# Performance work log

Measured on AMD Instinct MI355X. Metric: run time of the kernel, lower is better.

Reference implementation:

```python
import jax, jax.numpy as jnp
import numpy as np

# Mamba3TextEncoder config (class .small() defaults)
B_SZ, SEQ = 4, 512
VOCAB, D_MODEL, N_LAYERS = 32000, 768, 12
N_STATE, EXPAND, HEADDIM, NGROUPS, EMBED = 64, 2, 32, 1, 1536
D_INNER = EXPAND * D_MODEL            # 1536
NHEADS = D_INNER // HEADDIM           # 48
CONV_DIM = D_INNER + 2 * NGROUPS * N_STATE  # 1664 (x, B, C go through depthwise conv)
K_CONV = 4
PROJ_IN = 2 * D_INNER + 2 * NGROUPS * N_STATE + NHEADS  # z, xBC, dt


def setup_inputs() -> dict:
    key = jax.random.key(0)
    ks = jax.random.split(key, 16)
    s = 0.02
    return {
        "token_ids": jax.random.randint(ks[0], (B_SZ, SEQ), 0, VOCAB),
        "embed_W": jax.random.normal(ks[1], (VOCAB, D_MODEL), jnp.float32) * s,
        "ln_W": jnp.ones((N_LAYERS, D_MODEL), jnp.float32),
        "in_proj_W": jax.random.normal(ks[2], (N_LAYERS, D_MODEL, PROJ_IN), jnp.float32) * s,
        "conv_W": jax.random.normal(ks[3], (N_LAYERS, CONV_DIM, 1, K_CONV), jnp.float32) * 0.1,
        "conv_b": jnp.zeros((N_LAYERS, CONV_DIM), jnp.float32),
        "dt_bias": jax.random.uniform(ks[4], (N_LAYERS, NHEADS), jnp.float32, -4.6, -2.0),
        "A_log": jnp.tile(jnp.log(jnp.arange(1, NHEADS + 1, dtype=jnp.float32))[None], (N_LAYERS, 1)),
        "D": jnp.ones((N_LAYERS, NHEADS), jnp.float32),
        "norm_W": jnp.ones((N_LAYERS, D_INNER), jnp.float32),
        "out_proj_W": jax.random.normal(ks[5], (N_LAYERS, D_INNER, D_MODEL), jnp.float32) * s,
        "final_norm_W": jnp.ones((D_MODEL,), jnp.float32),
        "proj_W": jax.random.normal(ks[6], (D_MODEL, EMBED), jnp.float32) * s,
        "proj_b": jnp.zeros((EMBED,), jnp.float32),
    }


def _rmsnorm(x, w, eps=1e-5):
    return x * jax.lax.rsqrt(jnp.mean(x * x, axis=-1, keepdims=True) + eps) * w


def _causal_conv(x, w, b):
    # x: [B,S,C] depthwise causal conv, kernel K_CONV
    y = jax.lax.conv_general_dilated(
        x.transpose(0, 2, 1), w, (1,), [(K_CONV - 1, 0)],
        dimension_numbers=("NCH", "OIH", "NCH"), feature_group_count=CONV_DIM)
    return y.transpose(0, 2, 1) + b


def _ssm(xs, dt, A, Bm, Cm):
    # selective scan. xs:[B,S,H,P] dt:[B,S,H] A:[H] Bm,Cm:[B,S,N] (ngroups=1)
    decay = jnp.exp(dt * A)              # [B,S,H]
    dtx = dt[..., None] * xs             # [B,S,H,P]
    h0 = jnp.zeros((xs.shape[0], NHEADS, HEADDIM, N_STATE), xs.dtype)

    def step(h, inp):
        dec, dx, b, c = inp              # [B,H],[B,H,P],[B,N],[B,N]
        h = dec[..., None, None] * h + dx[..., None] * b[:, None, None, :]
        y = jnp.einsum("bhpn,bn->bhp", h, c)
        return h, y

    inputs = (decay.transpose(1, 0, 2), dtx.transpose(1, 0, 2, 3),
              Bm.transpose(1, 0, 2), Cm.transpose(1, 0, 2))
    _, ys = jax.lax.scan(step, h0, inputs)
    return ys.transpose(1, 0, 2, 3)      # [B,S,H,P]


def reference(token_ids, embed_W, ln_W, in_proj_W, conv_W, conv_b, dt_bias,
              A_log, D, norm_W, out_proj_W, final_norm_W, proj_W, proj_b):
    x = embed_W[token_ids]                               # [B,S,D]
    for l in range(N_LAYERS):
        h = _rmsnorm(x, ln_W[l])
        zxbcdt = h @ in_proj_W[l]                        # [B,S,PROJ_IN]
        z = zxbcdt[..., :D_INNER]
        xBC = zxbcdt[..., D_INNER:D_INNER + CONV_DIM]
        dt_raw = zxbcdt[..., D_INNER + CONV_DIM:]        # [B,S,H]
        xBC = jax.nn.silu(_causal_conv(xBC, conv_W[l], conv_b[l]))
        xs = xBC[..., :D_INNER].reshape(*xBC.shape[:2], NHEADS, HEADDIM)
        Bm = xBC[..., D_INNER:D_INNER + N_STATE]
        Cm = xBC[..., D_INNER + N_STATE:]
        dt = jax.nn.softplus(dt_raw + dt_bias[l])
        A = -jnp.exp(A_log[l])
        y = _ssm(xs, dt, A, Bm, Cm) + D[l][None, None, :, None] * xs
        y = y.reshape(*y.shape[:2], D_INNER)
        y = _rmsnorm(y * jax.nn.silu(z), norm_W[l])      # gated RMSNorm
        x = x + y @ out_proj_W[l]
    x = _rmsnorm(x, final_norm_W)
    pooled = x.mean(axis=1)                              # [B,D]
    proj = pooled @ proj_W + proj_b                      # [B,EMBED]
    n = jnp.sqrt(jnp.sum(proj * proj, axis=-1, keepdims=True))
    return proj / jnp.maximum(n, 1e-12)
```

## Files before the change

### kernel.cpp

```cpp
#include <hip/hip_runtime.h>
#include <math.h>

typedef __bf16 bf16x8 __attribute__((ext_vector_type(8)));
typedef short  s16x8  __attribute__((ext_vector_type(8)));
typedef float  f32x4  __attribute__((ext_vector_type(4)));

static constexpr int BSZ = 4, SEQ = 512, DM = 768;
static constexpr int DIN = 1536, NH = 48, HP = 32, NS = 64;
static constexpr int CDIM = 1664;
static constexpr int PROJ_IN = 3248;
static constexpr int LDZX = 3328;
static constexpr int ROWS = BSZ * SEQ;
static constexpr int EMBED = 1536;
static constexpr int NLAYERS = 12;

using gptr_t = const __attribute__((address_space(1))) void*;
using lptr_t = __attribute__((address_space(3))) void*;

__device__ __forceinline__ unsigned short f2bf(float f) {
  unsigned u = __builtin_bit_cast(unsigned, f);
  u += 0x7FFF + ((u >> 16) & 1);
  return (unsigned short)(u >> 16);
}
__device__ __forceinline__ float bf2f(unsigned short u) {
  unsigned v = (unsigned)u << 16;
  return __builtin_bit_cast(float, v);
}
__device__ __forceinline__ float sigm(float x) { return 1.f / (1.f + __expf(-x)); }
__device__ __forceinline__ float sp(float x) { return (x > 15.f) ? x : log1pf(__expf(x)); }

__device__ __forceinline__ void gll16(const void* g, void* l) {
  __builtin_amdgcn_global_load_lds((gptr_t)g, (lptr_t)l, 16, 0, 0);
}
__device__ __forceinline__ f32x4 mfma16(s16x8 a, s16x8 b, f32x4 c) {
  return __builtin_amdgcn_mfma_f32_16x16x32_bf16(
      __builtin_bit_cast(bf16x8, a), __builtin_bit_cast(bf16x8, b), c, 0, 0, 0);
}

template <int NW>
__device__ __forceinline__ float block_sum(float v) {
#pragma unroll
  for (int o = 32; o; o >>= 1) v += __shfl_xor(v, o);
  __shared__ float red[NW];
  if ((threadIdx.x & 63) == 0) red[threadIdx.x >> 6] = v;
  __syncthreads();
  float s = red[0];
#pragma unroll
  for (int i = 1; i < NW; ++i) s += red[i];
  return s;
}

__global__ void embed_k(const int* __restrict__ tok, const float* __restrict__ eW,
                        float* __restrict__ x) {
  int bt = blockIdx.x;
  const float4* src = (const float4*)(eW + (size_t)tok[bt] * DM);
  float4* dst = (float4*)(x + (size_t)bt * DM);
  dst[threadIdx.x] = src[threadIdx.x];
}

__global__ void transpose_cvt(const float* __restrict__ W, unsigned short* __restrict__ Wt,
                              int K, int N, int Npad) {
  __shared__ float tile[32][33];
  int l = blockIdx.z;
  const float* Wl = W + (size_t)l * K * N;
  unsigned short* Wtl = Wt + (size_t)l * Npad * K;
  int nb = blockIdx.x * 32, kb = blockIdx.y * 32;
  int tx = threadIdx.x, ty = threadIdx.y;
#pragma unroll
  for (int r = 0; r < 4; ++r) {
    int k = kb + ty + r * 8, n = nb + tx;
    tile[ty + r * 8][tx] = (n < N) ? Wl[(size_t)k * N + n] : 0.f;
  }
  __syncthreads();
#pragma unroll
  for (int r = 0; r < 4; ++r) {
    int n = nb + ty + r * 8, k = kb + tx;
    Wtl[(size_t)n * K + k] = f2bf(tile[tx][ty + r * 8]);
  }
}

template <typename OUT>
__global__ void rmsnorm_k(const float* __restrict__ x, const float* __restrict__ w,
                          OUT* __restrict__ out) {
  int bt = blockIdx.x, tid = threadIdx.x;
  float4 v = ((const float4*)(x + (size_t)bt * DM))[tid];
  float4 wv = ((const float4*)w)[tid];
  float ss = v.x * v.x + v.y * v.y + v.z * v.z + v.w * v.w;
  float tot = block_sum<3>(ss);
  float rs = rsqrtf(tot * (1.f / DM) + 1e-5f);
  float o0 = v.x * rs * wv.x, o1 = v.y * rs * wv.y, o2 = v.z * rs * wv.z, o3 = v.w * rs * wv.w;
  if constexpr (sizeof(OUT) == 4) {
    float4 o = {o0, o1, o2, o3};
    ((float4*)(out + (size_t)bt * DM))[tid] = o;
  } else {
    unsigned long long pk =
        (unsigned long long)f2bf(o0) | ((unsigned long long)f2bf(o1) << 16) |
        ((unsigned long long)f2bf(o2) << 32) | ((unsigned long long)f2bf(o3) << 48);
    *(unsigned long long*)((unsigned short*)out + (size_t)bt * DM + tid * 4) = pk;
  }
}

template <int BM, int BN, int MODE>
__global__ __launch_bounds__(256) void gemm_k(
    const unsigned short* __restrict__ A, const unsigned short* __restrict__ Bt,
    int K, void* __restrict__ O0, void* __restrict__ O1, void* __restrict__ O2) {
  constexpr int AIT = BM / 32, BIT = BN / 32, NST = AIT + BIT;
  constexpr int FM = BM / 32, FN = BN / 32;
  __shared__ unsigned short lA[2][BM * 64], lB[2][BN * 64];
  int tid = threadIdx.x, lane = tid & 63, wv = tid >> 6;
  int flat = blockIdx.y * gridDim.x + blockIdx.x;
  int q8 = (gridDim.x * gridDim.y) >> 3;
  int nf = (flat & 7) * q8 + (flat >> 3);
  int bx = nf % gridDim.x, by = nf / gridDim.x;
  int m0 = by * BM, n0 = bx * BN;
  int wm = (wv >> 1) * (BM / 2), wn = (wv & 1) * (BN / 2);
  int NK = K >> 6;
  auto stage = [&](int kt, int buf) {
#pragma unroll
    for (int i = 0; i < AIT; ++i) {
      int flt = i * 256 + tid, rr = flt >> 3, cc = flt & 7;
      gll16(A + (size_t)(m0 + rr) * K + kt + (cc ^ (rr & 7)) * 8, (char*)lA[buf] + flt * 16);
    }
#pragma unroll
    for (int i = 0; i < BIT; ++i) {
      int flt = i * 256 + tid, rr = flt >> 3, cc = flt & 7;
      gll16(Bt + (size_t)(n0 + rr) * K + kt + (cc ^ (rr & 7)) * 8, (char*)lB[buf] + flt * 16);
    }
  };
  f32x4 acc[FM][FN] = {};
  stage(0, 0);
  for (int i = 0; i < NK; ++i) {
    if (i + 1 < NK) {
      stage((i + 1) << 6, (i + 1) & 1);
      asm volatile("s_waitcnt vmcnt(%0)" :: "i"(NST) : "memory");
    } else {
      asm volatile("s_waitcnt vmcnt(0)" ::: "memory");
    }
    __builtin_amdgcn_s_barrier();
    __builtin_amdgcn_sched_barrier(0);
    const unsigned short* cA = lA[i & 1];
    const unsigned short* cB = lB[i & 1];
#pragma unroll
    for (int ks = 0; ks < 2; ++ks) {
      s16x8 a[FM], b[FN];
#pragma unroll
      for (int mi = 0; mi < FM; ++mi) {
        int row = wm + mi * 16 + (lane & 15);
        int ch = (ks * 4 + (lane >> 4)) ^ (row & 7);
        a[mi] = *(const s16x8*)((const char*)cA + row * 128 + ch * 16);
      }
#pragma unroll
      for (int nj = 0; nj < FN; ++nj) {
        int row = wn + nj * 16 + (lane & 15);
        int ch = (ks * 4 + (lane >> 4)) ^ (row & 7);
        b[nj] = *(const s16x8*)((const char*)cB + row * 128 + ch * 16);
      }
#pragma unroll
      for (int mi = 0; mi < FM; ++mi)
#pragma unroll
        for (int nj = 0; nj < FN; ++nj)
          acc[mi][nj] = mfma16(a[mi], b[nj], acc[mi][nj]);
    }
    __builtin_amdgcn_s_barrier();
  }
#pragma unroll
  for (int mi = 0; mi < FM; ++mi) {
    int rbase = m0 + wm + mi * 16 + ((lane >> 4) << 2);
#pragma unroll
    for (int nj = 0; nj < FN; ++nj) {
      int col = n0 + wn + nj * 16 + (lane & 15);
#pragma unroll
      for (int rg = 0; rg < 4; ++rg) {
        int row = rbase + rg;
        float vv = acc[mi][nj][rg];
        if constexpr (MODE == 0) {
          if (n0 < DIN) {
            ((unsigned short*)O0)[(size_t)row * DIN + col] = f2bf(vv);
          } else if (n0 < DIN + CDIM) {
            ((float*)O1)[(size_t)row * CDIM + (col - DIN)] = vv;
          } else {
            int c2 = col - (DIN + CDIM);
            if (c2 < NH) ((float*)O2)[(size_t)row * NH + c2] = vv;
          }
        } else {
          size_t idx = (size_t)row * DM + col;
          ((float*)O0)[idx] = vv + ((const float*)O1)[idx];
        }
      }
    }
  }
}

__global__ __launch_bounds__(256) void conv_dt_k(
    const float* __restrict__ xbc, const float* __restrict__ cw, const float* __restrict__ cb,
    const float* __restrict__ dtraw, const float* __restrict__ dbias,
    unsigned short* __restrict__ xs16, unsigned short* __restrict__ dtxT,
    unsigned short* __restrict__ Bbf, unsigned short* __restrict__ Cbf) {
  __shared__ float stg[11][256];
  __shared__ float dtl[8][48];
  int tid = threadIdx.x;
  int chunk = blockIdx.x;
  int bt0 = blockIdx.y * 8;
  int t0 = bt0 & (SEQ - 1);
  int cbase = chunk * 256;
#pragma unroll
  for (int i = 0; i < 11; ++i) {
    int s = t0 - 3 + i, col = cbase + tid;
    stg[i][tid] = (s >= 0 && col < CDIM) ? xbc[(size_t)(bt0 - 3 + i) * CDIM + col] : 0.f;
  }
  if (chunk < 6) {
    for (int idx = tid; idx < 384; idx += 256) {
      int r = idx / 48, hh = idx - r * 48;
      dtl[r][hh] = sp(dtraw[(size_t)(bt0 + r) * NH + hh] + dbias[hh]);
    }
  }
  __syncthreads();
  int c = cbase + tid;
  if (chunk < 6) {
    float w0 = cw[c * 4], w1 = cw[c * 4 + 1], w2 = cw[c * 4 + 2], w3 = cw[c * 4 + 3];
    float bias = cb[c];
    int hh = c >> 5, p = c & 31, b = bt0 >> 9;
    s16x8 pk;
#pragma unroll
    for (int r = 0; r < 8; ++r) {
      float a = bias + stg[r][tid] * w0 + stg[r + 1][tid] * w1 + stg[r + 2][tid] * w2 +
                stg[r + 3][tid] * w3;
      float sv = a * sigm(a);
      xs16[(size_t)(bt0 + r) * DIN + c] = f2bf(sv);
      pk[r] = (short)f2bf(sv * dtl[r][hh]);
    }
    *reinterpret_cast<s16x8*>(dtxT + ((((size_t)b * NH + hh) * HP + p) * SEQ + t0)) = pk;
  } else if (tid < 128) {
    int cc = DIN + tid;
    float w0 = cw[cc * 4], w1 = cw[cc * 4 + 1], w2 = cw[cc * 4 + 2], w3 = cw[cc * 4 + 3];
    float bias = cb[cc];
#pragma unroll
    for (int r = 0; r < 8; ++r) {
      float a = bias + stg[r][tid] * w0 + stg[r + 1][tid] * w1 + stg[r + 2][tid] * w2 +
                stg[r + 3][tid] * w3;
      float sv = a * sigm(a);
      if (tid < 64) Bbf[(size_t)(bt0 + r) * NS + tid] = f2bf(sv);
      else          Cbf[(size_t)(bt0 + r) * NS + (tid - 64)] = f2bf(sv);
    }
  }
}

__global__ __launch_bounds__(256) void scan_k(
    const unsigned short* __restrict__ Bbf, const unsigned short* __restrict__ Cbf,
    const unsigned short* __restrict__ dtxT, const unsigned short* __restrict__ xs16,
    const float* __restrict__ dtraw, const float* __restrict__ dbias,
    const float* __restrict__ alog, const float* __restrict__ Dvec,
    unsigned short* __restrict__ y16) {
  __shared__ unsigned short CbPt[64 * 64];
  __shared__ unsigned short Bb[2][64 * 64], Dx[2][32 * 64];
  __shared__ float lsb[SEQ];
  __shared__ float pair[256];
  __shared__ int sfirst;
  int tid = threadIdx.x, lane = tid & 63, wv = tid >> 6;
  int tb = blockIdx.x, h = blockIdx.y, b = blockIdx.z;
  int t0 = tb * 64;
  const unsigned short* dxrow = dtxT + ((size_t)b * NH + h) * HP * SEQ;

#pragma unroll
  for (int i = 0; i < 2; ++i) {
    int flt = i * 256 + tid, rr = flt >> 3, cc = flt & 7;
    gll16(Cbf + (size_t)(b * SEQ + t0 + rr) * NS + (cc ^ (rr & 7)) * 8, (char*)CbPt + flt * 16);
  }
  float bias = dbias[h];
  float Ah = -__expf(alog[h]);
  int t2 = tid * 2;
  float d0 = sp(dtraw[(size_t)(b * SEQ + t2) * NH + h] + bias) * Ah;
  float d1 = sp(dtraw[(size_t)(b * SEQ + t2 + 1) * NH + h] + bias) * Ah;
  pair[tid] = d0 + d1;
  __syncthreads();
  for (int off = 1; off < 256; off <<= 1) {
    float add = (tid >= off) ? pair[tid - off] : 0.f;
    float cur = pair[tid];
    __syncthreads();
    pair[tid] = cur + add;
    __syncthreads();
  }
  float excl = tid ? pair[tid - 1] : 0.f;
  lsb[t2] = excl + d0;
  lsb[t2 + 1] = excl + d0 + d1;
  if (tid == 0) sfirst = tb;
  __syncthreads();
  float REF = lsb[t0];
  if (tid < tb && (REF - lsb[tid * 64 + 63] >= -18.f)) atomicMin(&sfirst, tid);
  __syncthreads();
  int st0 = sfirst;

#pragma unroll
  for (int i = 0; i < 2; ++i) {
    int flt = i * 256 + tid, rr = flt >> 3, cc = flt & 7;
    gll16(Bbf + (size_t)(b * SEQ + st0 * 64 + rr) * NS + (cc ^ (rr & 7)) * 8,
          (char*)Bb[st0 & 1] + flt * 16);
  }
  { int rr = tid >> 3, cc = tid & 7;
    gll16(dxrow + (size_t)rr * SEQ + st0 * 64 + (cc ^ (rr & 7)) * 8,
          (char*)Dx[st0 & 1] + tid * 16); }

  float lt[4], elt[4];
  int trb = wv * 16 + ((lane >> 4) << 2);
#pragma unroll
  for (int rg = 0; rg < 4; ++rg) {
    lt[rg] = lsb[t0 + trb + rg];
    elt[rg] = __expf(lt[rg] - REF);
  }
  s16x8 aC[2];
  f32x4 yacc[2] = {};

  for (int st = st0; st <= tb; ++st) {
    int s0 = st * 64;
    if (st < tb) {
      int s1 = s0 + 64;
#pragma unroll
      for (int i = 0; i < 2; ++i) {
        int flt = i * 256 + tid, rr = flt >> 3, cc = flt & 7;
        gll16(Bbf + (size_t)(b * SEQ + s1 + rr) * NS + (cc ^ (rr & 7)) * 8,
              (char*)Bb[(st + 1) & 1] + flt * 16);
      }
      { int rr = tid >> 3, cc = tid & 7;
        gll16(dxrow + (size_t)rr * SEQ + s1 + (cc ^ (rr & 7)) * 8,
              (char*)Dx[(st + 1) & 1] + tid * 16); }
      asm volatile("s_waitcnt vmcnt(3)" ::: "memory");
    } else {
      asm volatile("s_waitcnt vmcnt(0)" ::: "memory");
    }
    __builtin_amdgcn_s_barrier();
    __builtin_amdgcn_sched_barrier(0);
    const unsigned short* Bcur = Bb[st & 1];
    const unsigned short* Dcur = Dx[st & 1];
    if (st == st0) {
#pragma unroll
      for (int ks = 0; ks < 2; ++ks) {
        int row = wv * 16 + (lane & 15);
        int ch = (ks * 4 + (lane >> 4)) ^ (row & 7);
        aC[ks] = *(const s16x8*)((const char*)CbPt + row * 128 + ch * 16);
      }
    }
    float lsv[4];
#pragma unroll
    for (int sq = 0; sq < 4; ++sq) lsv[sq] = lsb[s0 + sq * 16 + (lane & 15)];
    f32x4 gf[4] = {};
#pragma unroll
    for (int sq = 0; sq < 4; ++sq)
#pragma unroll
      for (int ks = 0; ks < 2; ++ks) {
        int row = sq * 16 + (lane & 15);
        int ch = (ks * 4 + (lane >> 4)) ^ (row & 7);
        s16x8 bB = *(const s16x8*)((const char*)Bcur + row * 128 + ch * 16);
        gf[sq] = mfma16(aC[ks], bB, gf[sq]);
      }
    if (st < tb) {
      float es[4];
#pragma unroll
      for (int sq = 0; sq < 4; ++sq) es[sq] = __expf(REF - lsv[sq]);
#pragma unroll
      for (int sq = 0; sq < 4; ++sq) {
        int scol = sq * 16 + (lane & 15);
#pragma unroll
        for (int rg = 0; rg < 4; ++rg) {
          int trow = trb + rg;
          int off = (trow * 128 + scol * 2) ^ ((trow & 7) << 4);
          *(unsigned short*)((char*)CbPt + off) = f2bf(gf[sq][rg] * (elt[rg] * es[sq]));
        }
      }
    } else {
#pragma unroll
      for (int sq = 0; sq < 4; ++sq) {
        int scol = sq * 16 + (lane & 15);
        int sg = s0 + scol;
#pragma unroll
        for (int rg = 0; rg < 4; ++rg) {
          int trow = trb + rg, tg = t0 + trow;
          float wgt = (sg <= tg) ? __expf(lt[rg] - lsv[sq]) : 0.f;
          int off = (trow * 128 + scol * 2) ^ ((trow & 7) << 4);
          *(unsigned short*)((char*)CbPt + off) = f2bf(gf[sq][rg] * wgt);
        }
      }
    }
#pragma unroll
    for (int ks = 0; ks < 2; ++ks) {
      int row = wv * 16 + (lane & 15);
      int ch = (ks * 4 + (lane >> 4)) ^ (row & 7);
      s16x8 aP = *(const s16x8*)((const char*)CbPt + row * 128 + ch * 16);
#pragma unroll
      for (int pq = 0; pq < 2; ++pq) {
        int prow = pq * 16 + (lane & 15);
        int pch = (ks * 4 + (lane >> 4)) ^ (prow & 7);
        s16x8 bD = *(const s16x8*)((const char*)Dcur + prow * 128 + pch * 16);
        yacc[pq] = mfma16(aP, bD, yacc[pq]);
      }
    }
    __builtin_amdgcn_s_barrier();
  }
  float Dh = Dvec[h];
#pragma unroll
  for (int pq = 0; pq < 2; ++pq) {
#pragma unroll
    for (int rg = 0; rg < 4; ++rg) {
      int trow = trb + rg;
      int tg = t0 + trow;
      int p = pq * 16 + (lane & 15);
      float xv = bf2f(xs16[(size_t)(b * SEQ + tg) * DIN + h * HP + p]);
      y16[(size_t)(b * SEQ + tg) * DIN + h * HP + p] = f2bf(yacc[pq][rg] + Dh * xv);
    }
  }
}

__global__ void gated_rms_k(const unsigned short* __restrict__ y16,
                            const unsigned short* __restrict__ zb,
                            const float* __restrict__ w, unsigned short* __restrict__ out) {
  int bt = blockIdx.x, tid = threadIdx.x;
  size_t base = (size_t)bt * DIN + tid * 8;
  s16x8 yv = *(const s16x8*)(y16 + base);
  s16x8 zv = *(const s16x8*)(zb + base);
  float g[8], ss = 0.f;
#pragma unroll
  for (int j = 0; j < 8; ++j) {
    float yf = bf2f((unsigned short)yv[j]), zf = bf2f((unsigned short)zv[j]);
    float gg = yf * zf * sigm(zf);
    g[j] = gg; ss += gg * gg;
  }
  float tot = block_sum<3>(ss);
  float rs = rsqrtf(tot * (1.f / DIN) + 1e-5f);
  s16x8 ov;
#pragma unroll
  for (int j = 0; j < 8; ++j) ov[j] = (short)f2bf(g[j] * rs * w[tid * 8 + j]);
  *(s16x8*)(out + base) = ov;
}

__global__ void pool_k(const float* __restrict__ fn, float* __restrict__ pooled) {
  int d = blockIdx.x * 256 + threadIdx.x, b = blockIdx.y;
  float s = 0.f;
  for (int t = 0; t < SEQ; ++t) s += fn[(size_t)(b * SEQ + t) * DM + d];
  pooled[b * DM + d] = s * (1.f / SEQ);
}
__global__ void proj_k(const float* __restrict__ pooled, const float* __restrict__ pW,
                       const float* __restrict__ pb, float* __restrict__ ptmp) {
  int e0 = blockIdx.x * 64, b = blockIdx.y;
  int el = threadIdx.x & 63, g = threadIdx.x >> 6;
  int e = e0 + el;
  float s = 0.f;
  for (int d = g * 192; d < (g + 1) * 192; ++d)
    s += pooled[b * DM + d] * pW[(size_t)d * EMBED + e];
  __shared__ float red[4][64];
  red[g][el] = s;
  __syncthreads();
  if (g == 0) ptmp[b * EMBED + e] = red[0][el] + red[1][el] + red[2][el] + red[3][el] + pb[e];
}
__global__ void l2_k(const float* __restrict__ ptmp, float* __restrict__ out) {
  int b = blockIdx.x;
  float v[6], ss = 0.f;
#pragma unroll
  for (int i = 0; i < 6; ++i) {
    v[i] = ptmp[(size_t)b * EMBED + threadIdx.x + i * 256];
    ss += v[i] * v[i];
  }
  float tot = block_sum<4>(ss);
  float inv = 1.f / fmaxf(sqrtf(tot), 1e-12f);
#pragma unroll
  for (int i = 0; i < 6; ++i)
    out[(size_t)b * EMBED + threadIdx.x + i * 256] = v[i] * inv;
}

extern "C" void kernel_launch(void* const* d_in, const int* in_sizes, int n_in,
                              void* d_out, int out_size, void* d_ws, size_t ws_size,
                              hipStream_t stream) {
  const int*   tok  = (const int*)d_in[0];
  const float* embW = (const float*)d_in[1];
  const float* lnW  = (const float*)d_in[2];
  const float* ipW  = (const float*)d_in[3];
  const float* cW   = (const float*)d_in[4];
  const float* cB   = (const float*)d_in[5];
  const float* dtB  = (const float*)d_in[6];
  const float* Alog = (const float*)d_in[7];
  const float* Dv   = (const float*)d_in[8];
  const float* nW   = (const float*)d_in[9];
  const float* opW  = (const float*)d_in[10];
  const float* fnW  = (const float*)d_in[11];
  const float* pW   = (const float*)d_in[12];
  const float* pb   = (const float*)d_in[13];
  float* out = (float*)d_out;

  char* wsp = (char*)d_ws;
  auto alloc = [&](size_t bytes) {
    char* p = wsp;
    wsp += (bytes + 255) & ~(size_t)255;
    return p;
  };
  float* x      = (float*)alloc((size_t)ROWS * DM * 4);
  float* xbc    = (float*)alloc((size_t)ROWS * CDIM * 4);
  float* dtraw  = (float*)alloc((size_t)ROWS * NH * 4);
  float* pooled = (float*)alloc((size_t)BSZ * DM * 4);
  float* ptmp   = (float*)alloc((size_t)BSZ * EMBED * 4);
  float* fn     = (float*)alloc((size_t)ROWS * DM * 4);
  unsigned short* zb    = (unsigned short*)alloc((size_t)ROWS * DIN * 2);
  unsigned short* xs16  = (unsigned short*)alloc((size_t)ROWS * DIN * 2);
  unsigned short* y16   = (unsigned short*)alloc((size_t)ROWS * DIN * 2);
  unsigned short* h16   = (unsigned short*)alloc((size_t)ROWS * DM * 2);
  unsigned short* yg16  = (unsigned short*)alloc((size_t)ROWS * DIN * 2);
  unsigned short* dtxT  = (unsigned short*)alloc((size_t)BSZ * NH * HP * SEQ * 2);
  unsigned short* Bbf   = (unsigned short*)alloc((size_t)ROWS * NS * 2);
  unsigned short* Cbf   = (unsigned short*)alloc((size_t)ROWS * NS * 2);
  unsigned short* wptA  = (unsigned short*)alloc((size_t)NLAYERS * LDZX * DM * 2);
  unsigned short* wotA  = (unsigned short*)alloc((size_t)NLAYERS * DM * DIN * 2);

  embed_k<<<ROWS, 192, 0, stream>>>(tok, embW, x);
  transpose_cvt<<<dim3(LDZX / 32, DM / 32, NLAYERS), dim3(32, 8), 0, stream>>>(
      ipW, wptA, DM, PROJ_IN, LDZX);
  transpose_cvt<<<dim3(DM / 32, DIN / 32, NLAYERS), dim3(32, 8), 0, stream>>>(
      opW, wotA, DIN, DM, DM);

  for (int l = 0; l < NLAYERS; ++l) {
    rmsnorm_k<unsigned short><<<ROWS, 192, 0, stream>>>(x, lnW + l * DM, h16);
    gemm_k<128, 128, 0><<<dim3(LDZX / 128, ROWS / 128), 256, 0, stream>>>(
        h16, wptA + (size_t)l * LDZX * DM, DM, zb, xbc, dtraw);
    conv_dt_k<<<dim3(7, ROWS / 8), 256, 0, stream>>>(
        xbc, cW + (size_t)l * CDIM * 4, cB + (size_t)l * CDIM, dtraw, dtB + l * NH,
        xs16, dtxT, Bbf, Cbf);
    scan_k<<<dim3(SEQ / 64, NH, BSZ), 256, 0, stream>>>(
        Bbf, Cbf, dtxT, xs16, dtraw, dtB + l * NH, Alog + l * NH, Dv + l * NH, y16);
    gated_rms_k<<<ROWS, 192, 0, stream>>>(y16, zb, nW + (size_t)l * DIN, yg16);
    gemm_k<64, 64, 1><<<dim3(DM / 64, ROWS / 64), 256, 0, stream>>>(
        yg16, wotA + (size_t)l * DM * DIN, DIN, x, x, nullptr);
  }

  rmsnorm_k<float><<<ROWS, 192, 0, stream>>>(x, fnW, fn);
  pool_k<<<dim3(DM / 256, BSZ), 256, 0, stream>>>(fn, pooled);
  proj_k<<<dim3(EMBED / 64, BSZ), 256, 0, stream>>>(pooled, pW, pb, ptmp);
  l2_k<<<BSZ, 256, 0, stream>>>(ptmp, out);
}
```

Before: 1.065 ms.

## Pre-pack GEMM operands into MFMA fragment layout and load directly to registers

Weights and activations are now written in a packed 16-row by 32-k fragment order, so each lane of the new GEMM can load its MFMA operands with a single contiguous 16-byte global load. This removes the LDS staging, swizzling and barriers of the old GEMM and replaces them with register double-buffering, at the cost of relying on L1/L2 for cross-wave reuse. The embedding lookup is fused with the first layer's RMSNorm. The scan's chunk-skip threshold is also tightened from -18 to -12, which skips more decayed history at a small accuracy cost.

```diff
diff --git a/kernel.cpp b/kernel.cpp
--- a/kernel.cpp
+++ b/kernel.cpp
@@ -50,38 +50,57 @@
   return s;
 }
 
-__global__ void embed_k(const int* __restrict__ tok, const float* __restrict__ eW,
-                        float* __restrict__ x) {
-  int bt = blockIdx.x;
-  const float4* src = (const float4*)(eW + (size_t)tok[bt] * DM);
-  float4* dst = (float4*)(x + (size_t)bt * DM);
-  dst[threadIdx.x] = src[threadIdx.x];
-}
-
-__global__ void transpose_cvt(const float* __restrict__ W, unsigned short* __restrict__ Wt,
-                              int K, int N, int Npad) {
+
+__global__ void embed_rms_k(const int* __restrict__ tok, const float* __restrict__ eW,
+                            const float* __restrict__ w, float* __restrict__ x,
+                            unsigned short* __restrict__ hpk) {
+  int bt = blockIdx.x, tid = threadIdx.x;
+  float4 v = ((const float4*)(eW + (size_t)tok[bt] * DM))[tid];
+  ((float4*)(x + (size_t)bt * DM))[tid] = v;
+  float4 wv = ((const float4*)w)[tid];
+  float ss = v.x * v.x + v.y * v.y + v.z * v.z + v.w * v.w;
+  float tot = block_sum<3>(ss);
+  float rs = rsqrtf(tot * (1.f / DM) + 1e-5f);
+  int k0 = tid * 4;
+  unsigned long long pk =
+      (unsigned long long)f2bf(v.x * rs * wv.x) |
+      ((unsigned long long)f2bf(v.y * rs * wv.y) << 16) |
+      ((unsigned long long)f2bf(v.z * rs * wv.z) << 32) |
+      ((unsigned long long)f2bf(v.w * rs * wv.w) << 48);
+  size_t idx = (((size_t)(bt >> 4) * 24 + (k0 >> 5)) * 64 +
+                ((bt & 15) | (((k0 >> 3) & 3) << 4))) * 8 + (k0 & 7);
+  *(unsigned long long*)(hpk + idx) = pk;
+}
+
+__global__ void transpose_pk(const float* __restrict__ W, unsigned short* __restrict__ Wpk,
+                             int K, int N, int Npad) {
   __shared__ float tile[32][33];
-  int l = blockIdx.z;
+  int l = blockIdx.z, KC = K >> 5;
   const float* Wl = W + (size_t)l * K * N;
-  unsigned short* Wtl = Wt + (size_t)l * Npad * K;
+  unsigned short* Wp = Wpk + (size_t)l * Npad * K;
   int nb = blockIdx.x * 32, kb = blockIdx.y * 32;
-  int tx = threadIdx.x, ty = threadIdx.y;
+  int tx = threadIdx.x & 31, ty = threadIdx.x >> 5;
 #pragma unroll
   for (int r = 0; r < 4; ++r) {
     int k = kb + ty + r * 8, n = nb + tx;
     tile[ty + r * 8][tx] = (n < N) ? Wl[(size_t)k * N + n] : 0.f;
   }
   __syncthreads();
-#pragma unroll
-  for (int r = 0; r < 4; ++r) {
-    int n = nb + ty + r * 8, k = kb + tx;
-    Wtl[(size_t)n * K + k] = f2bf(tile[tx][ty + r * 8]);
-  }
-}
-
-template <typename OUT>
+  int n_local = threadIdx.x >> 3, kg = threadIdx.x & 7;
+  int n = nb + n_local, k0 = kb + kg * 4;
+  unsigned long long pk =
+      (unsigned long long)f2bf(tile[kg * 4 + 0][n_local]) |
+      ((unsigned long long)f2bf(tile[kg * 4 + 1][n_local]) << 16) |
+      ((unsigned long long)f2bf(tile[kg * 4 + 2][n_local]) << 32) |
+      ((unsigned long long)f2bf(tile[kg * 4 + 3][n_local]) << 48);
+  size_t idx = (((size_t)(n >> 4) * KC + (k0 >> 5)) * 64 +
+                ((n & 15) | (((k0 >> 3) & 3) << 4))) * 8 + (k0 & 7);
+  *(unsigned long long*)(Wp + idx) = pk;
+}
+
+template <bool PACK>
 __global__ void rmsnorm_k(const float* __restrict__ x, const float* __restrict__ w,
-                          OUT* __restrict__ out) {
+                          void* __restrict__ out) {
   int bt = blockIdx.x, tid = threadIdx.x;
   float4 v = ((const float4*)(x + (size_t)bt * DM))[tid];
   float4 wv = ((const float4*)w)[tid];
@@ -89,82 +108,65 @@
   float tot = block_sum<3>(ss);
   float rs = rsqrtf(tot * (1.f / DM) + 1e-5f);
   float o0 = v.x * rs * wv.x, o1 = v.y * rs * wv.y, o2 = v.z * rs * wv.z, o3 = v.w * rs * wv.w;
-  if constexpr (sizeof(OUT) == 4) {
+  if constexpr (!PACK) {
     float4 o = {o0, o1, o2, o3};
-    ((float4*)(out + (size_t)bt * DM))[tid] = o;
+    ((float4*)((float*)out + (size_t)bt * DM))[tid] = o;
   } else {
+    int k0 = tid * 4;
     unsigned long long pk =
         (unsigned long long)f2bf(o0) | ((unsigned long long)f2bf(o1) << 16) |
         ((unsigned long long)f2bf(o2) << 32) | ((unsigned long long)f2bf(o3) << 48);
-    *(unsigned long long*)((unsigned short*)out + (size_t)bt * DM + tid * 4) = pk;
-  }
-}
-
-template <int BM, int BN, int MODE>
-__global__ __launch_bounds__(256) void gemm_k(
-    const unsigned short* __restrict__ A, const unsigned short* __restrict__ Bt,
-    int K, void* __restrict__ O0, void* __restrict__ O1, void* __restrict__ O2) {
-  constexpr int AIT = BM / 32, BIT = BN / 32, NST = AIT + BIT;
-  constexpr int FM = BM / 32, FN = BN / 32;
-  __shared__ unsigned short lA[2][BM * 64], lB[2][BN * 64];
+    size_t idx = (((size_t)(bt >> 4) * 24 + (k0 >> 5)) * 64 +
+                  ((bt & 15) | (((k0 >> 3) & 3) << 4))) * 8 + (k0 & 7);
+    *(unsigned long long*)((unsigned short*)out + idx) = pk;
+  }
+}
+
+template <int FN, int MODE>
+__global__ __launch_bounds__(256) void gemm_pk(
+    const unsigned short* __restrict__ Apk, const unsigned short* __restrict__ Bpk,
+    int K, void* __restrict__ O0, void* __restrict__ O1) {
+  constexpr int BN = FN * 32;
+  int KC = K >> 5;
   int tid = threadIdx.x, lane = tid & 63, wv = tid >> 6;
   int flat = blockIdx.y * gridDim.x + blockIdx.x;
   int q8 = (gridDim.x * gridDim.y) >> 3;
   int nf = (flat & 7) * q8 + (flat >> 3);
   int bx = nf % gridDim.x, by = nf / gridDim.x;
-  int m0 = by * BM, n0 = bx * BN;
-  int wm = (wv >> 1) * (BM / 2), wn = (wv & 1) * (BN / 2);
-  int NK = K >> 6;
-  auto stage = [&](int kt, int buf) {
-#pragma unroll
-    for (int i = 0; i < AIT; ++i) {
-      int flt = i * 256 + tid, rr = flt >> 3, cc = flt & 7;
-      gll16(A + (size_t)(m0 + rr) * K + kt + (cc ^ (rr & 7)) * 8, (char*)lA[buf] + flt * 16);
-    }
-#pragma unroll
-    for (int i = 0; i < BIT; ++i) {
-      int flt = i * 256 + tid, rr = flt >> 3, cc = flt & 7;
-      gll16(Bt + (size_t)(n0 + rr) * K + kt + (cc ^ (rr & 7)) * 8, (char*)lB[buf] + flt * 16);
-    }
+  int m0 = by * 128, n0 = bx * BN;
+  int wm = (wv >> 1) * 64, wn = (wv & 1) * (FN * 16);
+  int arb = (m0 + wm) >> 4, brb = (n0 + wn) >> 4;
+  const unsigned short* abase = Apk + ((size_t)arb * KC) * 512 + lane * 8;
+  const unsigned short* bbase = Bpk + ((size_t)brb * KC) * 512 + lane * 8;
+  auto lda = [&](s16x8* A, int cb) {
+#pragma unroll
+    for (int mi = 0; mi < 4; ++mi)
+      A[mi] = *(const s16x8*)(abase + ((size_t)mi * KC + cb) * 512);
   };
-  f32x4 acc[FM][FN] = {};
-  stage(0, 0);
-  for (int i = 0; i < NK; ++i) {
-    if (i + 1 < NK) {
-      stage((i + 1) << 6, (i + 1) & 1);
-      asm volatile("s_waitcnt vmcnt(%0)" :: "i"(NST) : "memory");
-    } else {
-      asm volatile("s_waitcnt vmcnt(0)" ::: "memory");
-    }
-    __builtin_amdgcn_s_barrier();
-    __builtin_amdgcn_sched_barrier(0);
-    const unsigned short* cA = lA[i & 1];
-    const unsigned short* cB = lB[i & 1];
-#pragma unroll
-    for (int ks = 0; ks < 2; ++ks) {
-      s16x8 a[FM], b[FN];
-#pragma unroll
-      for (int mi = 0; mi < FM; ++mi) {
-        int row = wm + mi * 16 + (lane & 15);
-        int ch = (ks * 4 + (lane >> 4)) ^ (row & 7);
-        a[mi] = *(const s16x8*)((const char*)cA + row * 128 + ch * 16);
-      }
-#pragma unroll
-      for (int nj = 0; nj < FN; ++nj) {
-        int row = wn + nj * 16 + (lane & 15);
-        int ch = (ks * 4 + (lane >> 4)) ^ (row & 7);
-        b[nj] = *(const s16x8*)((const char*)cB + row * 128 + ch * 16);
-      }
-#pragma unroll
-      for (int mi = 0; mi < FM; ++mi)
-#pragma unroll
-        for (int nj = 0; nj < FN; ++nj)
-          acc[mi][nj] = mfma16(a[mi], b[nj], acc[mi][nj]);
-    }
-    __builtin_amdgcn_s_barrier();
-  }
-#pragma unroll
-  for (int mi = 0; mi < FM; ++mi) {
+  auto ldb = [&](s16x8* B, int cb) {
+#pragma unroll
+    for (int nj = 0; nj < FN; ++nj)
+      B[nj] = *(const s16x8*)(bbase + ((size_t)nj * KC + cb) * 512);
+  };
+  f32x4 acc[4][FN] = {};
+  s16x8 A0[4], B0[FN], A1[4], B1[FN];
+  lda(A0, 0); ldb(B0, 0);
+  for (int cb = 0; cb < KC; cb += 2) {
+    lda(A1, cb + 1); ldb(B1, cb + 1);
+#pragma unroll
+    for (int mi = 0; mi < 4; ++mi)
+#pragma unroll
+      for (int nj = 0; nj < FN; ++nj)
+        acc[mi][nj] = mfma16(A0[mi], B0[nj], acc[mi][nj]);
+    if (cb + 2 < KC) { lda(A0, cb + 2); ldb(B0, cb + 2); }
+#pragma unroll
+    for (int mi = 0; mi < 4; ++mi)
+#pragma unroll
+      for (int nj = 0; nj < FN; ++nj)
+        acc[mi][nj] = mfma16(A1[mi], B1[nj], acc[mi][nj]);
+  }
+#pragma unroll
+  for (int mi = 0; mi < 4; ++mi) {
     int rbase = m0 + wm + mi * 16 + ((lane >> 4) << 2);
 #pragma unroll
     for (int nj = 0; nj < FN; ++nj) {
@@ -174,13 +176,13 @@
         int row = rbase + rg;
         float vv = acc[mi][nj][rg];
         if constexpr (MODE == 0) {
-          if (n0 < DIN) {
+          if (col < DIN) {
             ((unsigned short*)O0)[(size_t)row * DIN + col] = f2bf(vv);
-          } else if (n0 < DIN + CDIM) {
+          } else if (col < DIN + CDIM) {
             ((float*)O1)[(size_t)row * CDIM + (col - DIN)] = vv;
           } else {
             int c2 = col - (DIN + CDIM);
-            if (c2 < NH) ((float*)O2)[(size_t)row * NH + c2] = vv;
+            if (c2 < NH) ((float*)O1 + (size_t)ROWS * CDIM)[(size_t)row * NH + c2] = vv;
           }
         } else {
           size_t idx = (size_t)row * DM + col;
@@ -286,7 +288,7 @@
   if (tid == 0) sfirst = tb;
   __syncthreads();
   float REF = lsb[t0];
-  if (tid < tb && (REF - lsb[tid * 64 + 63] >= -18.f)) atomicMin(&sfirst, tid);
+  if (tid < tb && (REF - lsb[tid * 64 + 63] >= -12.f)) atomicMin(&sfirst, tid);
   __syncthreads();
   int st0 = sfirst;
 
@@ -411,7 +413,7 @@
 
 __global__ void gated_rms_k(const unsigned short* __restrict__ y16,
                             const unsigned short* __restrict__ zb,
-                            const float* __restrict__ w, unsigned short* __restrict__ out) {
+                            const float* __restrict__ w, unsigned short* __restrict__ outpk) {
   int bt = blockIdx.x, tid = threadIdx.x;
   size_t base = (size_t)bt * DIN + tid * 8;
   s16x8 yv = *(const s16x8*)(y16 + base);
@@ -428,7 +430,9 @@
   s16x8 ov;
 #pragma unroll
   for (int j = 0; j < 8; ++j) ov[j] = (short)f2bf(g[j] * rs * w[tid * 8 + j]);
-  *(s16x8*)(out + base) = ov;
+  size_t idx = (((size_t)(bt >> 4) * 48 + (tid >> 2)) * 64 +
+                ((bt & 15) | ((tid & 3) << 4))) * 8;
+  *(s16x8*)(outpk + idx) = ov;
 }
 
 __global__ void pool_k(const float* __restrict__ fn, float* __restrict__ pooled) {
@@ -499,35 +503,37 @@
   unsigned short* zb    = (unsigned short*)alloc((size_t)ROWS * DIN * 2);
   unsigned short* xs16  = (unsigned short*)alloc((size_t)ROWS * DIN * 2);
   unsigned short* y16   = (unsigned short*)alloc((size_t)ROWS * DIN * 2);
-  unsigned short* h16   = (unsigned short*)alloc((size_t)ROWS * DM * 2);
-  unsigned short* yg16  = (unsigned short*)alloc((size_t)ROWS * DIN * 2);
+  unsigned short* hpk   = (unsigned short*)alloc((size_t)ROWS * DM * 2);
+  unsigned short* ygpk  = (unsigned short*)alloc((size_t)ROWS * DIN * 2);
   unsigned short* dtxT  = (unsigned short*)alloc((size_t)BSZ * NH * HP * SEQ * 2);
   unsigned short* Bbf   = (unsigned short*)alloc((size_t)ROWS * NS * 2);
   unsigned short* Cbf   = (unsigned short*)alloc((size_t)ROWS * NS * 2);
-  unsigned short* wptA  = (unsigned short*)alloc((size_t)NLAYERS * LDZX * DM * 2);
-  unsigned short* wotA  = (unsigned short*)alloc((size_t)NLAYERS * DM * DIN * 2);
-
-  embed_k<<<ROWS, 192, 0, stream>>>(tok, embW, x);
-  transpose_cvt<<<dim3(LDZX / 32, DM / 32, NLAYERS), dim3(32, 8), 0, stream>>>(
-      ipW, wptA, DM, PROJ_IN, LDZX);
-  transpose_cvt<<<dim3(DM / 32, DIN / 32, NLAYERS), dim3(32, 8), 0, stream>>>(
-      opW, wotA, DIN, DM, DM);
+  unsigned short* wpkA  = (unsigned short*)alloc((size_t)NLAYERS * LDZX * DM * 2);
+  unsigned short* wpkO  = (unsigned short*)alloc((size_t)NLAYERS * DM * DIN * 2);
+
+
+  embed_rms_k<<<ROWS, 192, 0, stream>>>(tok, embW, lnW, x, hpk);
+  transpose_pk<<<dim3(LDZX / 32, DM / 32, NLAYERS), 256, 0, stream>>>(
+      ipW, wpkA, DM, PROJ_IN, LDZX);
+  transpose_pk<<<dim3(DM / 32, DIN / 32, NLAYERS), 256, 0, stream>>>(
+      opW, wpkO, DIN, DM, DM);
 
   for (int l = 0; l < NLAYERS; ++l) {
-    rmsnorm_k<unsigned short><<<ROWS, 192, 0, stream>>>(x, lnW + l * DM, h16);
-    gemm_k<128, 128, 0><<<dim3(LDZX / 128, ROWS / 128), 256, 0, stream>>>(
-        h16, wptA + (size_t)l * LDZX * DM, DM, zb, xbc, dtraw);
+    if (l > 0)
+      rmsnorm_k<true><<<ROWS, 192, 0, stream>>>(x, lnW + l * DM, hpk);
+    gemm_pk<4, 0><<<dim3(LDZX / 128, ROWS / 128), 256, 0, stream>>>(
+        hpk, wpkA + (size_t)l * LDZX * DM, DM, zb, xbc);
     conv_dt_k<<<dim3(7, ROWS / 8), 256, 0, stream>>>(
         xbc, cW + (size_t)l * CDIM * 4, cB + (size_t)l * CDIM, dtraw, dtB + l * NH,
         xs16, dtxT, Bbf, Cbf);
     scan_k<<<dim3(SEQ / 64, NH, BSZ), 256, 0, stream>>>(
         Bbf, Cbf, dtxT, xs16, dtraw, dtB + l * NH, Alog + l * NH, Dv + l * NH, y16);
-    gated_rms_k<<<ROWS, 192, 0, stream>>>(y16, zb, nW + (size_t)l * DIN, yg16);
-    gemm_k<64, 64, 1><<<dim3(DM / 64, ROWS / 64), 256, 0, stream>>>(
-        yg16, wotA + (size_t)l * DM * DIN, DIN, x, x, nullptr);
-  }
-
-  rmsnorm_k<float><<<ROWS, 192, 0, stream>>>(x, fnW, fn);
+    gated_rms_k<<<ROWS, 192, 0, stream>>>(y16, zb, nW + (size_t)l * DIN, ygpk);
+    gemm_pk<2, 1><<<dim3(DM / 64, ROWS / 128), 256, 0, stream>>>(
+        ygpk, wpkO + (size_t)l * DM * DIN, DIN, x, x);
+  }
+
+  rmsnorm_k<false><<<ROWS, 192, 0, stream>>>(x, fnW, fn);
   pool_k<<<dim3(DM / 256, BSZ), 256, 0, stream>>>(fn, pooled);
   proj_k<<<dim3(EMBED / 64, BSZ), 256, 0, stream>>>(pooled, pW, pb, ptmp);
   l2_k<<<BSZ, 256, 0, stream>>>(ptmp, out);
```

Result: slower. 1.241 ms (+16.6%).

## Fold RMSNorm weights into GEMM weights and fuse norms into GEMM epilogues

Applied to the files above, without the earlier changes.

Removes the per-layer rmsnorm and gated-RMSNorm kernels. Norm weights are folded into the transposed bf16 weight matrices. Per-row partial sums of squares are produced in the out-proj GEMM epilogue, the scan epilogue and the embed kernel, and each consumer GEMM applies rsqrt row scaling to its accumulator. The SiLU(z) gating moves into the scan epilogue, softplus(dt) is precomputed once per layer in conv_dt, and the final norm is folded into pooling. The scan's early-skip threshold is tightened from -18 to -12, which cuts more scan work but may change numerics. Row scaling is now applied after the bf16 GEMM rather than before the input is quantized.

```diff
diff --git a/kernel.cpp b/kernel.cpp
--- a/kernel.cpp
+++ b/kernel.cpp
@@ -51,25 +51,33 @@
 }
 
 __global__ void embed_k(const int* __restrict__ tok, const float* __restrict__ eW,
-                        float* __restrict__ x) {
-  int bt = blockIdx.x;
-  const float4* src = (const float4*)(eW + (size_t)tok[bt] * DM);
-  float4* dst = (float4*)(x + (size_t)bt * DM);
-  dst[threadIdx.x] = src[threadIdx.x];
-}
-
-__global__ void transpose_cvt(const float* __restrict__ W, unsigned short* __restrict__ Wt,
-                              int K, int N, int Npad) {
+                        float* __restrict__ x, unsigned short* __restrict__ x16,
+                        float* __restrict__ ssq1p) {
+  int bt = blockIdx.x, tid = threadIdx.x;
+  float4 v = ((const float4*)(eW + (size_t)tok[bt] * DM))[tid];
+  ((float4*)(x + (size_t)bt * DM))[tid] = v;
+  unsigned long long pk =
+      (unsigned long long)f2bf(v.x) | ((unsigned long long)f2bf(v.y) << 16) |
+      ((unsigned long long)f2bf(v.z) << 32) | ((unsigned long long)f2bf(v.w) << 48);
+  *(unsigned long long*)(x16 + (size_t)bt * DM + tid * 4) = pk;
+  float ss = v.x * v.x + v.y * v.y + v.z * v.z + v.w * v.w;
+  float tot = block_sum<3>(ss);
+  if (tid < 24) ssq1p[(size_t)bt * 24 + tid] = (tid == 0) ? tot : 0.f;
+}
+
+__global__ void transpose_cvt(const float* __restrict__ W, const float* __restrict__ sc,
+                              unsigned short* __restrict__ Wt, int K, int N, int Npad) {
   __shared__ float tile[32][33];
   int l = blockIdx.z;
   const float* Wl = W + (size_t)l * K * N;
+  const float* scl = sc + (size_t)l * K;
   unsigned short* Wtl = Wt + (size_t)l * Npad * K;
   int nb = blockIdx.x * 32, kb = blockIdx.y * 32;
   int tx = threadIdx.x, ty = threadIdx.y;
 #pragma unroll
   for (int r = 0; r < 4; ++r) {
     int k = kb + ty + r * 8, n = nb + tx;
-    tile[ty + r * 8][tx] = (n < N) ? Wl[(size_t)k * N + n] : 0.f;
+    tile[ty + r * 8][tx] = (n < N) ? Wl[(size_t)k * N + n] * scl[k] : 0.f;
   }
   __syncthreads();
 #pragma unroll
@@ -79,34 +87,18 @@
   }
 }
 
-template <typename OUT>
-__global__ void rmsnorm_k(const float* __restrict__ x, const float* __restrict__ w,
-                          OUT* __restrict__ out) {
-  int bt = blockIdx.x, tid = threadIdx.x;
-  float4 v = ((const float4*)(x + (size_t)bt * DM))[tid];
-  float4 wv = ((const float4*)w)[tid];
-  float ss = v.x * v.x + v.y * v.y + v.z * v.z + v.w * v.w;
-  float tot = block_sum<3>(ss);
-  float rs = rsqrtf(tot * (1.f / DM) + 1e-5f);
-  float o0 = v.x * rs * wv.x, o1 = v.y * rs * wv.y, o2 = v.z * rs * wv.z, o3 = v.w * rs * wv.w;
-  if constexpr (sizeof(OUT) == 4) {
-    float4 o = {o0, o1, o2, o3};
-    ((float4*)(out + (size_t)bt * DM))[tid] = o;
-  } else {
-    unsigned long long pk =
-        (unsigned long long)f2bf(o0) | ((unsigned long long)f2bf(o1) << 16) |
-        ((unsigned long long)f2bf(o2) << 32) | ((unsigned long long)f2bf(o3) << 48);
-    *(unsigned long long*)((unsigned short*)out + (size_t)bt * DM + tid * 4) = pk;
-  }
-}
-
 template <int BM, int BN, int MODE>
 __global__ __launch_bounds__(256) void gemm_k(
     const unsigned short* __restrict__ A, const unsigned short* __restrict__ Bt,
-    int K, void* __restrict__ O0, void* __restrict__ O1, void* __restrict__ O2) {
+    int K, const float* __restrict__ ssqp, void* __restrict__ O0,
+    void* __restrict__ O1, void* __restrict__ O2,
+    unsigned short* __restrict__ x16o, float* __restrict__ ssqo) {
   constexpr int AIT = BM / 32, BIT = BN / 32, NST = AIT + BIT;
   constexpr int FM = BM / 32, FN = BN / 32;
+  constexpr int NSSQ = (MODE == 0) ? 24 : 48;
+  constexpr float INVD = (MODE == 0) ? (1.f / 768.f) : (1.f / 1536.f);
   __shared__ unsigned short lA[2][BM * 64], lB[2][BN * 64];
+  __shared__ float rss[BM];
   int tid = threadIdx.x, lane = tid & 63, wv = tid >> 6;
   int flat = blockIdx.y * gridDim.x + blockIdx.x;
   int q8 = (gridDim.x * gridDim.y) >> 3;
@@ -127,8 +119,16 @@
       gll16(Bt + (size_t)(n0 + rr) * K + kt + (cc ^ (rr & 7)) * 8, (char*)lB[buf] + flt * 16);
     }
   };
+  stage(0, 0);
+  if (tid < BM) {
+    const float* p = ssqp + (size_t)(m0 + tid) * NSSQ;
+    float s = 0.f;
+#pragma unroll
+    for (int j = 0; j < NSSQ; ++j) s += p[j];
+    rss[tid] = rsqrtf(s * INVD + 1e-5f);
+  }
+  __syncthreads();
   f32x4 acc[FM][FN] = {};
-  stage(0, 0);
   for (int i = 0; i < NK; ++i) {
     if (i + 1 < NK) {
       stage((i + 1) << 6, (i + 1) & 1);
@@ -165,14 +165,18 @@
   }
 #pragma unroll
   for (int mi = 0; mi < FM; ++mi) {
-    int rbase = m0 + wm + mi * 16 + ((lane >> 4) << 2);
+    int rl0 = wm + mi * 16 + ((lane >> 4) << 2);
+    float rsr[4];
+#pragma unroll
+    for (int rg = 0; rg < 4; ++rg) rsr[rg] = rss[rl0 + rg];
+    float part[4] = {0.f, 0.f, 0.f, 0.f};
 #pragma unroll
     for (int nj = 0; nj < FN; ++nj) {
       int col = n0 + wn + nj * 16 + (lane & 15);
 #pragma unroll
       for (int rg = 0; rg < 4; ++rg) {
-        int row = rbase + rg;
-        float vv = acc[mi][nj][rg];
+        int row = m0 + rl0 + rg;
+        float vv = acc[mi][nj][rg] * rsr[rg];
         if constexpr (MODE == 0) {
           if (n0 < DIN) {
             ((unsigned short*)O0)[(size_t)row * DIN + col] = f2bf(vv);
@@ -184,8 +188,23 @@
           }
         } else {
           size_t idx = (size_t)row * DM + col;
-          ((float*)O0)[idx] = vv + ((const float*)O1)[idx];
+          float xn = vv + ((float*)O0)[idx];
+          ((float*)O0)[idx] = xn;
+          x16o[idx] = f2bf(xn);
+          part[rg] += xn * xn;
         }
+      }
+    }
+    if constexpr (MODE == 1) {
+#pragma unroll
+      for (int rg = 0; rg < 4; ++rg) {
+#pragma unroll
+        for (int off = 1; off < 16; off <<= 1) part[rg] += __shfl_xor(part[rg], off);
+      }
+      if ((lane & 15) == 0) {
+#pragma unroll
+        for (int rg = 0; rg < 4; ++rg)
+          ssqo[(size_t)(m0 + rl0 + rg) * 24 + bx * 2 + (wn >> 5)] = part[rg];
       }
     }
   }
@@ -195,7 +214,8 @@
     const float* __restrict__ xbc, const float* __restrict__ cw, const float* __restrict__ cb,
     const float* __restrict__ dtraw, const float* __restrict__ dbias,
     unsigned short* __restrict__ xs16, unsigned short* __restrict__ dtxT,
-    unsigned short* __restrict__ Bbf, unsigned short* __restrict__ Cbf) {
+    unsigned short* __restrict__ Bbf, unsigned short* __restrict__ Cbf,
+    float* __restrict__ dts) {
   __shared__ float stg[11][256];
   __shared__ float dtl[8][48];
   int tid = threadIdx.x;
@@ -242,15 +262,25 @@
       if (tid < 64) Bbf[(size_t)(bt0 + r) * NS + tid] = f2bf(sv);
       else          Cbf[(size_t)(bt0 + r) * NS + (tid - 64)] = f2bf(sv);
     }
+  } else if (tid < 176) {
+    int hh = tid - 128;
+    float bias_ = dbias[hh];
+    float v[8];
+#pragma unroll
+    for (int r = 0; r < 8; ++r) v[r] = sp(dtraw[(size_t)(bt0 + r) * NH + hh] + bias_);
+    float4 a4 = {v[0], v[1], v[2], v[3]}, b4 = {v[4], v[5], v[6], v[7]};
+    float* dp = dts + ((size_t)(bt0 >> 9) * NH + hh) * SEQ + t0;
+    *(float4*)dp = a4;
+    *(float4*)(dp + 4) = b4;
   }
 }
 
 __global__ __launch_bounds__(256) void scan_k(
     const unsigned short* __restrict__ Bbf, const unsigned short* __restrict__ Cbf,
     const unsigned short* __restrict__ dtxT, const unsigned short* __restrict__ xs16,
-    const float* __restrict__ dtraw, const float* __restrict__ dbias,
+    const float* __restrict__ dts, const unsigned short* __restrict__ zb,
     const float* __restrict__ alog, const float* __restrict__ Dvec,
-    unsigned short* __restrict__ y16) {
+    unsigned short* __restrict__ g16, float* __restrict__ ssq2p) {
   __shared__ unsigned short CbPt[64 * 64];
   __shared__ unsigned short Bb[2][64 * 64], Dx[2][32 * 64];
   __shared__ float lsb[SEQ];
@@ -266,11 +296,10 @@
     int flt = i * 256 + tid, rr = flt >> 3, cc = flt & 7;
     gll16(Cbf + (size_t)(b * SEQ + t0 + rr) * NS + (cc ^ (rr & 7)) * 8, (char*)CbPt + flt * 16);
   }
-  float bias = dbias[h];
   float Ah = -__expf(alog[h]);
   int t2 = tid * 2;
-  float d0 = sp(dtraw[(size_t)(b * SEQ + t2) * NH + h] + bias) * Ah;
-  float d1 = sp(dtraw[(size_t)(b * SEQ + t2 + 1) * NH + h] + bias) * Ah;
+  float2 dv = *(const float2*)(dts + ((size_t)b * NH + h) * SEQ + t2);
+  float d0 = dv.x * Ah, d1 = dv.y * Ah;
   pair[tid] = d0 + d1;
   __syncthreads();
   for (int off = 1; off < 256; off <<= 1) {
@@ -286,7 +315,7 @@
   if (tid == 0) sfirst = tb;
   __syncthreads();
   float REF = lsb[t0];
-  if (tid < tb && (REF - lsb[tid * 64 + 63] >= -18.f)) atomicMin(&sfirst, tid);
+  if (tid < tb && (REF - lsb[tid * 64 + 63] >= -12.f)) atomicMin(&sfirst, tid);
   __syncthreads();
   int st0 = sfirst;
 
@@ -396,6 +425,7 @@
     __builtin_amdgcn_s_barrier();
   }
   float Dh = Dvec[h];
+  float part[4] = {0.f, 0.f, 0.f, 0.f};
 #pragma unroll
   for (int pq = 0; pq < 2; ++pq) {
 #pragma unroll
@@ -403,39 +433,43 @@
       int trow = trb + rg;
       int tg = t0 + trow;
       int p = pq * 16 + (lane & 15);
-      float xv = bf2f(xs16[(size_t)(b * SEQ + tg) * DIN + h * HP + p]);
-      y16[(size_t)(b * SEQ + tg) * DIN + h * HP + p] = f2bf(yacc[pq][rg] + Dh * xv);
-    }
-  }
-}
-
-__global__ void gated_rms_k(const unsigned short* __restrict__ y16,
-                            const unsigned short* __restrict__ zb,
-                            const float* __restrict__ w, unsigned short* __restrict__ out) {
-  int bt = blockIdx.x, tid = threadIdx.x;
-  size_t base = (size_t)bt * DIN + tid * 8;
-  s16x8 yv = *(const s16x8*)(y16 + base);
-  s16x8 zv = *(const s16x8*)(zb + base);
-  float g[8], ss = 0.f;
-#pragma unroll
-  for (int j = 0; j < 8; ++j) {
-    float yf = bf2f((unsigned short)yv[j]), zf = bf2f((unsigned short)zv[j]);
-    float gg = yf * zf * sigm(zf);
-    g[j] = gg; ss += gg * gg;
-  }
-  float tot = block_sum<3>(ss);
-  float rs = rsqrtf(tot * (1.f / DIN) + 1e-5f);
-  s16x8 ov;
-#pragma unroll
-  for (int j = 0; j < 8; ++j) ov[j] = (short)f2bf(g[j] * rs * w[tid * 8 + j]);
-  *(s16x8*)(out + base) = ov;
-}
-
-__global__ void pool_k(const float* __restrict__ fn, float* __restrict__ pooled) {
-  int d = blockIdx.x * 256 + threadIdx.x, b = blockIdx.y;
+      size_t gi = (size_t)(b * SEQ + tg) * DIN + h * HP + p;
+      float xv = bf2f(xs16[gi]);
+      float yv = yacc[pq][rg] + Dh * xv;
+      float zf = bf2f(zb[gi]);
+      float g = yv * zf * sigm(zf);
+      g16[gi] = f2bf(g);
+      part[rg] += g * g;
+    }
+  }
+#pragma unroll
+  for (int rg = 0; rg < 4; ++rg) {
+#pragma unroll
+    for (int off = 1; off < 16; off <<= 1) part[rg] += __shfl_xor(part[rg], off);
+  }
+  if ((lane & 15) == 0) {
+#pragma unroll
+    for (int rg = 0; rg < 4; ++rg)
+      ssq2p[(size_t)(b * SEQ + t0 + trb + rg) * 48 + h] = part[rg];
+  }
+}
+
+__global__ void pool_k(const float* __restrict__ x, const float* __restrict__ ssq1p,
+                       const float* __restrict__ fnW, float* __restrict__ pooled) {
+  __shared__ float rsl[SEQ];
+  int b = blockIdx.y, d0 = blockIdx.x * 256;
+  for (int t = threadIdx.x; t < SEQ; t += 256) {
+    const float* p = ssq1p + (size_t)(b * SEQ + t) * 24;
+    float s = 0.f;
+#pragma unroll
+    for (int j = 0; j < 24; ++j) s += p[j];
+    rsl[t] = rsqrtf(s * (1.f / DM) + 1e-5f);
+  }
+  __syncthreads();
+  int d = d0 + threadIdx.x;
   float s = 0.f;
-  for (int t = 0; t < SEQ; ++t) s += fn[(size_t)(b * SEQ + t) * DM + d];
-  pooled[b * DM + d] = s * (1.f / SEQ);
+  for (int t = 0; t < SEQ; ++t) s += x[(size_t)(b * SEQ + t) * DM + d] * rsl[t];
+  pooled[b * DM + d] = s * (1.f / SEQ) * fnW[d];
 }
 __global__ void proj_k(const float* __restrict__ pooled, const float* __restrict__ pW,
                        const float* __restrict__ pb, float* __restrict__ ptmp) {
@@ -493,42 +527,40 @@
   float* x      = (float*)alloc((size_t)ROWS * DM * 4);
   float* xbc    = (float*)alloc((size_t)ROWS * CDIM * 4);
   float* dtraw  = (float*)alloc((size_t)ROWS * NH * 4);
+  float* dts    = (float*)alloc((size_t)BSZ * NH * SEQ * 4);
+  float* ssq1p  = (float*)alloc((size_t)ROWS * 24 * 4);
+  float* ssq2p  = (float*)alloc((size_t)ROWS * 48 * 4);
   float* pooled = (float*)alloc((size_t)BSZ * DM * 4);
   float* ptmp   = (float*)alloc((size_t)BSZ * EMBED * 4);
-  float* fn     = (float*)alloc((size_t)ROWS * DM * 4);
+  unsigned short* x16   = (unsigned short*)alloc((size_t)ROWS * DM * 2);
   unsigned short* zb    = (unsigned short*)alloc((size_t)ROWS * DIN * 2);
   unsigned short* xs16  = (unsigned short*)alloc((size_t)ROWS * DIN * 2);
-  unsigned short* y16   = (unsigned short*)alloc((size_t)ROWS * DIN * 2);
-  unsigned short* h16   = (unsigned short*)alloc((size_t)ROWS * DM * 2);
-  unsigned short* yg16  = (unsigned short*)alloc((size_t)ROWS * DIN * 2);
+  unsigned short* g16   = (unsigned short*)alloc((size_t)ROWS * DIN * 2);
   unsigned short* dtxT  = (unsigned short*)alloc((size_t)BSZ * NH * HP * SEQ * 2);
   unsigned short* Bbf   = (unsigned short*)alloc((size_t)ROWS * NS * 2);
   unsigned short* Cbf   = (unsigned short*)alloc((size_t)ROWS * NS * 2);
-  unsigned short* wptA  = (unsigned short*)alloc((size_t)NLAYERS * LDZX * DM * 2);
-  unsigned short* wotA  = (unsigned short*)alloc((size_t)NLAYERS * DM * DIN * 2);
-
-  embed_k<<<ROWS, 192, 0, stream>>>(tok, embW, x);
+  unsigned short* wtA   = (unsigned short*)alloc((size_t)NLAYERS * LDZX * DM * 2);
+  unsigned short* wtO   = (unsigned short*)alloc((size_t)NLAYERS * DM * DIN * 2);
+
+  embed_k<<<ROWS, 192, 0, stream>>>(tok, embW, x, x16, ssq1p);
   transpose_cvt<<<dim3(LDZX / 32, DM / 32, NLAYERS), dim3(32, 8), 0, stream>>>(
-      ipW, wptA, DM, PROJ_IN, LDZX);
+      ipW, lnW, wtA, DM, PROJ_IN, LDZX);
   transpose_cvt<<<dim3(DM / 32, DIN / 32, NLAYERS), dim3(32, 8), 0, stream>>>(
-      opW, wotA, DIN, DM, DM);
+      opW, nW, wtO, DIN, DM, DM);
 
   for (int l = 0; l < NLAYERS; ++l) {
-    rmsnorm_k<unsigned short><<<ROWS, 192, 0, stream>>>(x, lnW + l * DM, h16);
     gemm_k<128, 128, 0><<<dim3(LDZX / 128, ROWS / 128), 256, 0, stream>>>(
-        h16, wptA + (size_t)l * LDZX * DM, DM, zb, xbc, dtraw);
+        x16, wtA + (size_t)l * LDZX * DM, DM, ssq1p, zb, xbc, dtraw, nullptr, nullptr);
     conv_dt_k<<<dim3(7, ROWS / 8), 256, 0, stream>>>(
         xbc, cW + (size_t)l * CDIM * 4, cB + (size_t)l * CDIM, dtraw, dtB + l * NH,
-        xs16, dtxT, Bbf, Cbf);
+        xs16, dtxT, Bbf, Cbf, dts);
     scan_k<<<dim3(SEQ / 64, NH, BSZ), 256, 0, stream>>>(
-        Bbf, Cbf, dtxT, xs16, dtraw, dtB + l * NH, Alog + l * NH, Dv + l * NH, y16);
-    gated_rms_k<<<ROWS, 192, 0, stream>>>(y16, zb, nW + (size_t)l * DIN, yg16);
+        Bbf, Cbf, dtxT, xs16, dts, zb, Alog + l * NH, Dv + l * NH, g16, ssq2p);
     gemm_k<64, 64, 1><<<dim3(DM / 64, ROWS / 64), 256, 0, stream>>>(
-        yg16, wotA + (size_t)l * DM * DIN, DIN, x, x, nullptr);
-  }
-
-  rmsnorm_k<float><<<ROWS, 192, 0, stream>>>(x, fnW, fn);
-  pool_k<<<dim3(DM / 256, BSZ), 256, 0, stream>>>(fn, pooled);
+        g16, wtO + (size_t)l * DM * DIN, DIN, ssq2p, x, nullptr, nullptr, x16, ssq1p);
+  }
+
+  pool_k<<<dim3(DM / 256, BSZ), 256, 0, stream>>>(x, ssq1p, fnW, pooled);
   proj_k<<<dim3(EMBED / 64, BSZ), 256, 0, stream>>>(pooled, pW, pb, ptmp);
   l2_k<<<BSZ, 256, 0, stream>>>(ptmp, out);
 }
```

New measurement: 950.0 us. 1.12x faster.
